# Kernel optimization log

Measured on AMD Instinct MI355X. Metric: run time of the kernel, lower is better.

Reference implementation:

```python
import jax, jax.numpy as jnp
import numpy as np

NUM_QUERIES = 150
NEG = 1e9


def setup_inputs() -> dict:
    key = jax.random.key(0)
    ks = jax.random.split(key, 5)
    B, C, H, W = 4, 256, 64, 64
    img_feat = jax.random.normal(ks[0], (B, C, H, W), dtype=jnp.float32)
    exe_feat = jax.random.normal(ks[1], (B, C), dtype=jnp.float32)
    mask = jax.random.bernoulli(ks[2], 0.9, (B, H, W)).astype(jnp.float32)
    # similarity initialized as identity (plus tiny noise so it's non-degenerate)
    similarity = jnp.eye(C, dtype=jnp.float32) + 0.01 * jax.random.normal(ks[3], (C, C), dtype=jnp.float32)
    # nn.Linear weight, shape (out, in)
    v_w = jax.random.normal(ks[4], (C, C), dtype=jnp.float32) / np.sqrt(C)
    return {"img_feat": img_feat, "exe_feat": exe_feat, "mask": mask,
            "similarity": similarity, "v_w": v_w}


def _get_queries(attn, B, H, W):
    # peak detection on similarity-to-exemplar channel (last column), no grad
    simil = jax.lax.stop_gradient(attn[:, :, -1]).reshape(B, H, W)
    c = simil[:, 1:-1, 1:-1]
    is_max = ((c > simil[:, :-2, 1:-1]) &   # strictly greater than above
              (c >= simil[:, 2:, 1:-1]) &   # >= below
              (c > simil[:, 1:-1, :-2]) &   # strictly greater than left
              (c >= simil[:, 1:-1, 2:]))    # >= right
    pen = jnp.zeros_like(simil).at[:, 1:-1, 1:-1].set(
        jnp.where(is_max, 0.0, NEG))
    scores = (simil - pen).reshape(B, H * W)
    _, q_ids = jax.lax.top_k(scores, NUM_QUERIES)  # [B, Q]
    return q_ids


def reference(img_feat, exe_feat, mask, similarity, v_w):
    B, C, H, W = img_feat.shape
    HW = H * W
    unrolled = img_feat.reshape(B, C, HW)                      # [B,C,HW]
    exe = (exe_feat * 1.2)[:, :, None]                         # [B,C,1]
    concat = jnp.concatenate([unrolled, exe], axis=2)          # [B,C,HW+1]
    # values = Linear(concat^T): x @ W^T
    values = jnp.einsum('bcn,dc->bnd', concat, v_w)            # [B,HW+1,C]
    # attn = unrolled^T @ similarity @ concat
    attn = jnp.einsum('bcn,cd,bdm->bnm', unrolled, similarity, concat)  # [B,HW,HW+1]

    q_ids = _get_queries(attn, B, H, W)                        # [B,Q] int
    queries = jnp.take_along_axis(values[:, :-1], q_ids[:, :, None], axis=1)  # [B,Q,C]

    # masked softmax: outer product of pixel mask, exemplar column always kept
    m = jax.lax.stop_gradient(mask).reshape(B, HW)
    mm = m[:, :, None] * m[:, None, :]                         # [B,HW,HW]
    mm = jnp.concatenate([mm, jnp.ones((B, HW, 1), mm.dtype)], axis=2)
    attn = attn - (mm != 1).astype(attn.dtype) * NEG
    attn = jax.nn.softmax(attn, axis=2)

    new_img = jnp.einsum('bnm,bmd->bnd', attn, values)         # [B,HW,C]
    new_img = new_img.transpose(0, 2, 1).reshape(B, C, H, W)
    return new_img + img_feat, queries
```

## Files before the change

kernel.cpp:

```cpp
#include <hip/hip_runtime.h>

#define CC   256
#define HWS  4096
#define MPAD 4160
#define NB   4
#define NTIL 65

typedef __attribute__((ext_vector_type(8))) short   short8;
typedef __attribute__((ext_vector_type(4))) float   floatx4;

static __device__ __forceinline__ short8 ld8(const unsigned short* p) {
  return *(const short8*)p;
}
static __device__ __forceinline__ void st8(unsigned short* p, short8 v) {
  *(short8*)p = v;
}
static __device__ __forceinline__ unsigned short f2b(float x) {
  union { float f; unsigned u; } v; v.f = x;
  unsigned r = v.u + 0x7FFFu + ((v.u >> 16) & 1u);
  return (unsigned short)(r >> 16);
}
static __device__ __forceinline__ float b2f(unsigned short x) {
  union { unsigned u; float f; } v; v.u = ((unsigned)x) << 16;
  return v.f;
}

__global__ void prep_colb(const float* __restrict__ sim, const float* __restrict__ vw,
                          const float* __restrict__ mask,
                          unsigned short* __restrict__ St, unsigned short* __restrict__ Vw,
                          float* __restrict__ colb) {
  int blk = blockIdx.x, tid = threadIdx.x;
  if (blk < CC) {
    int dd = blk, c = tid;
    St[dd*CC + c] = f2b(sim[c*CC + dd]);
    Vw[dd*CC + c] = f2b(vw[dd*CC + c]);
    return;
  }
  int b = blk - CC;
  for (int m = tid; m < MPAD; m += 256) {
    float v;
    if (m < HWS)      v = (mask[b*HWS + m] - 1.0f) * 1e9f;
    else if (m == HWS) v = 0.0f;
    else               v = -3.0e38f;
    colb[b*MPAD + m] = v;
  }
}

__global__ void build_kt(const float* __restrict__ img, const float* __restrict__ exe,
                         unsigned short* __restrict__ Kt, unsigned short* __restrict__ Kf) {
  int b = blockIdx.x, mt = blockIdx.y, dt = blockIdx.z;
  int tid = threadIdx.x;
  int m0 = mt*64, d0 = dt*64;
  int w = tid >> 6, lane = tid & 63, lo = lane & 15, hi = lane >> 4;
  unsigned short* kft = Kf + (size_t)(b*NTIL + mt)*16384;
  if (mt == 64) {
    for (int i = 0; i < 16; ++i) {
      int m = m0 + (tid>>6) + i*4;
      int d = d0 + (tid&63);
      unsigned short v = 0;
      if (m == 4096) v = f2b(1.2f * exe[b*CC + d]);
      Kt[((size_t)b*MPAD + m)*CC + d] = v;
    }
#pragma unroll
    for (int ss = 0; ss < 2; ++ss) {
      int s = dt*8 + w*2 + ss;
      int k = s >> 2, t = s & 3;
      unsigned short tmp[8] = {0,0,0,0,0,0,0,0};
      if (t == 0 && lo == 0) {
#pragma unroll
        for (int j = 0; j < 8; ++j)
          tmp[j] = f2b(1.2f * exe[b*CC + k*32 + hi*8 + j]);
      }
      st8(kft + s*512 + lane*8, *(short8*)tmp);
    }
    return;
  }
  __shared__ float tile[64][65];
  for (int i = 0; i < 16; ++i) {
    int dl = (tid>>6) + i*4, ml = tid&63;
    tile[dl][ml] = img[((size_t)b*CC + d0+dl)*HWS + m0+ml];
  }
  __syncthreads();
  for (int i = 0; i < 16; ++i) {
    int ml = (tid>>6) + i*4, dl = tid&63;
    Kt[((size_t)b*MPAD + m0+ml)*CC + d0+dl] = f2b(tile[dl][ml]);
  }
#pragma unroll
  for (int ss = 0; ss < 2; ++ss) {
    int s = dt*8 + w*2 + ss;
    int k = s >> 2, t = s & 3;
    int ml = t*16 + lo;
    int dlb = (k - dt*2)*32 + hi*8;
    unsigned short tmp[8];
#pragma unroll
    for (int j = 0; j < 8; ++j) tmp[j] = f2b(tile[dlb + j][ml]);
    st8(kft + s*512 + lane*8, *(short8*)tmp);
  }
}

__global__ __launch_bounds__(256) void gemm_small(const unsigned short* __restrict__ Kt,
    const unsigned short* __restrict__ Bm, unsigned short* __restrict__ Tout,
    unsigned short* __restrict__ Vf, int mode) {
  int b  = blockIdx.x;
  int by = blockIdx.y;
  int w  = threadIdx.x >> 6;
  int r0 = by*64 + w*16;
  int c0 = blockIdx.z*64;
  int lane = threadIdx.x & 63;
  int lo = lane & 15, hi = lane >> 4;
  __shared__ unsigned short lsh[64][72];
  floatx4 acc[4] = {};
  const unsigned short* arow = Kt + ((size_t)b*MPAD + r0 + lo)*CC + hi*8;
#pragma unroll
  for (int k = 0; k < 8; ++k) {
    short8 af = ld8(arow + k*32);
#pragma unroll
    for (int t = 0; t < 4; ++t) {
      short8 bf = ld8(Bm + (size_t)(c0 + t*16 + lo)*CC + k*32 + hi*8);
      acc[t] = __builtin_amdgcn_mfma_f32_16x16x32_bf16(af, bf, acc[t], 0, 0, 0);
    }
  }
  if (mode == 0) {
#pragma unroll
    for (int t = 0; t < 4; ++t)
#pragma unroll
      for (int r = 0; r < 4; ++r)
        lsh[w*16 + hi*4 + r][t*16 + lo] = f2b(acc[t][r]);
    __syncthreads();
    int tid = threadIdx.x;
    int nl = tid >> 2, seg = tid & 3;
    unsigned short* dst = Tout + ((size_t)b*HWS + by*64 + nl)*CC + c0 + seg*16;
    st8(dst,     ld8(&lsh[nl][seg*16]));
    st8(dst + 8, ld8(&lsh[nl][seg*16 + 8]));
  } else {
#pragma unroll
    for (int t = 0; t < 4; ++t)
#pragma unroll
      for (int r = 0; r < 4; ++r)
        lsh[t*16 + lo][w*16 + hi*4 + r] = f2b(acc[t][r]);
    __syncthreads();
    unsigned short* vfb2 = Vf + (size_t)(b*NTIL + by)*16384;
#pragma unroll
    for (int ss = 0; ss < 2; ++ss) {
      int idx = w*2 + ss;
      int h = idx >> 2, t4 = idx & 3;
      int s = h*16 + (c0 >> 4) + t4;
      short8 v = ld8(&lsh[t4*16 + (lane & 15)][h*32 + (lane >> 4)*8]);
      st8(vfb2 + s*512 + lane*8, v);
    }
  }
}

__global__ __launch_bounds__(256) void scores_kernel(const float* __restrict__ img,
    const float* __restrict__ sim, const float* __restrict__ exe,
    float* __restrict__ score32) {
  int b = blockIdx.x, n0 = blockIdx.y*32;
  int d = threadIdx.x;
  __shared__ float U[32][257];
  __shared__ float R[32][257];
  __shared__ float E[256];
  for (int idx = threadIdx.x; idx < 32*256; idx += 256) {
    int nl = idx & 31, c = idx >> 5;
    U[nl][c] = img[((size_t)b*CC + c)*HWS + n0 + nl];
  }
  E[d] = 1.2f * exe[b*CC + d];
  __syncthreads();
  float acc[32];
#pragma unroll
  for (int nl = 0; nl < 32; ++nl) acc[nl] = 0.f;
  for (int c = 0; c < CC; ++c) {
    float s_cd = sim[c*CC + d];
#pragma unroll
    for (int nl = 0; nl < 32; ++nl) acc[nl] = fmaf(U[nl][c], s_cd, acc[nl]);
  }
#pragma unroll
  for (int nl = 0; nl < 32; ++nl) R[nl][d] = acc[nl];
  __syncthreads();
  if (d < 32) {
    float s = 0.f;
    for (int dd = 0; dd < CC; ++dd) s = fmaf(R[d][dd], E[dd], s);
    score32[b*HWS + n0 + d] = s;
  }
}

__global__ __launch_bounds__(64) void select_kernel(const float* __restrict__ scores,
                                                    int* __restrict__ qids) {
  int b = blockIdx.x, lane = threadIdx.x;
  __shared__ float sc[HWS];
  __shared__ unsigned long long kx[HWS];
  __shared__ unsigned long long list[256];
  __shared__ unsigned int hist[256];
  __shared__ unsigned int st[4];
  __shared__ unsigned long long sh_base;

  const floatx4* s4 = (const floatx4*)(scores + (size_t)b*HWS);
  floatx4* c4 = (floatx4*)sc;
#pragma unroll
  for (int i = 0; i < 16; ++i) c4[i*64 + lane] = s4[i*64 + lane];
  __syncthreads();

  for (int i = 0; i < 64; ++i) {
    int idx = i*64 + lane;
    int y = i, x = lane;
    float c0 = sc[idx];
    float v = c0;
    if (y >= 1 && y <= 62 && x >= 1 && x <= 62) {
      bool ismax = (c0 > sc[idx-64]) && (c0 >= sc[idx+64]) &&
                   (c0 > sc[idx-1])  && (c0 >= sc[idx+1]);
      if (!ismax) v = c0 - 1e9f;
    }
    unsigned u = __float_as_uint(v);
    u = (u & 0x80000000u) ? ~u : (u | 0x80000000u);
    kx[idx] = (((unsigned long long)u) << 12) | (unsigned long long)(4095 - idx);
  }
  __syncthreads();

  unsigned long long base = 0;
  unsigned int need = 150, C = 0;
  for (int s = 36; s >= 4; s -= 8) {
    for (int i = lane; i < 256; i += 64) hist[i] = 0;
    __syncthreads();
    unsigned long long pref = base >> (s + 8);
    for (int i = 0; i < 64; ++i) {
      unsigned long long k = kx[i*64 + lane];
      if ((k >> (s + 8)) == pref) atomicAdd(&hist[(unsigned)(k >> s) & 255u], 1u);
    }
    __syncthreads();
    if (lane == 0) {
      unsigned cum = 0; int B = 0;
      for (int bin = 255; bin >= 0; --bin) {
        cum += hist[bin];
        if (cum >= need) { B = bin; break; }
      }
      st[0] = (150u - need) + cum;
      st[1] = need - (cum - hist[B]);
      sh_base = base | ((unsigned long long)B << s);
    }
    __syncthreads();
    C = st[0]; need = st[1]; base = sh_base;
    if (C <= 256u) break;
  }

  if (lane == 0) st[2] = 0;
  __syncthreads();
  for (int i = 0; i < 64; ++i) {
    unsigned long long k = kx[i*64 + lane];
    if (k >= base) {
      unsigned p = atomicAdd(&st[2], 1u);
      list[p] = k;
    }
  }
  __syncthreads();
  for (int i = lane; i < 256; i += 64) if (i >= (int)C) list[i] = 0ull;
  __syncthreads();

  for (int kk = 2; kk <= 256; kk <<= 1) {
    for (int j = kk >> 1; j > 0; j >>= 1) {
#pragma unroll
      for (int tt = 0; tt < 2; ++tt) {
        int t = lane + tt*64;
        int i2 = ((t & ~(j - 1)) << 1) | (t & (j - 1));
        int p2 = i2 | j;
        bool desc = ((i2 & kk) == 0);
        unsigned long long a = list[i2], c = list[p2];
        bool sw = desc ? (a < c) : (a > c);
        if (sw) { list[i2] = c; list[p2] = a; }
      }
      __syncthreads();
    }
  }

  for (int q = lane; q < 150; q += 64)
    qids[b*150 + q] = 4095 - (int)(list[q] & 0xFFFull);
}

__global__ __launch_bounds__(256, 1) void flash_kernel(
    const unsigned short* __restrict__ Tb, const unsigned short* __restrict__ Kt,
    const unsigned short* __restrict__ Kf, const unsigned short* __restrict__ Vf,
    const float* __restrict__ mask, const float* __restrict__ colb,
    float* __restrict__ acc0, float* __restrict__ accH, float* __restrict__ lsums) {
  int blk = blockIdx.x;
  int b    = (blk & 7) >> 1;
  int half = blk & 1;
  int g    = blk >> 3;
  int tid = threadIdx.x;
  int wave = tid >> 6, lane = tid & 63;
  int lo = lane & 15, hi = lane >> 4;
  int n0 = g*128 + wave*32;
  int t0 = half ? 33 : 0, t1 = half ? NTIL : 33;

  __shared__ unsigned short pbuf[4][1152];
  unsigned short* plw = &pbuf[wave][0];

  short8 q0[8], q1[8];
  const unsigned short* tb0 = Tb + ((size_t)b*HWS + n0 + lo)*CC + hi*8;
#pragma unroll
  for (int k = 0; k < 8; ++k) { q0[k] = ld8(tb0 + k*32); q1[k] = ld8(tb0 + 16*CC + k*32); }

  const unsigned short* kfb = Kf + (size_t)b*NTIL*16384 + lane*8;
  const unsigned short* vfb = Vf + (size_t)b*NTIL*16384 + lane*8;

  short8 X[16], Y[16];
#pragma unroll
  for (int i = 0; i < 16; ++i) X[i] = ld8(kfb + (size_t)t0*16384 + i*512);
#pragma unroll
  for (int i = 0; i < 16; ++i) Y[i] = ld8(kfb + (size_t)t0*16384 + (16 + i)*512);

  const float* mk = mask + b*HWS;

  float crb0[4], Msub0[4], crb1[4], Msub1[4];
  {
    const unsigned short* kep = Kt + ((size_t)b*MPAD + HWS)*CC + hi*8;
    float ddot = 0.f, edot = 0.f;
    const unsigned short* kdp = Kt + ((size_t)b*MPAD + n0 + lo)*CC + hi*8;
#pragma unroll
    for (int k = 0; k < 8; ++k) {
      short8 kd = ld8(kdp + k*32);
      short8 ke = ld8(kep + k*32);
#pragma unroll
      for (int j = 0; j < 8; ++j) {
        float qf = b2f((unsigned short)q0[k][j]);
        ddot = fmaf(qf, b2f((unsigned short)kd[j]), ddot);
        edot = fmaf(qf, b2f((unsigned short)ke[j]), edot);
      }
    }
    ddot += __shfl_xor(ddot, 16); ddot += __shfl_xor(ddot, 32);
    edot += __shfl_xor(edot, 16); edot += __shfl_xor(edot, 32);
    float Mrow = ((mk[n0 + lo] == 1.0f) ? ddot : edot) + 2.0f;
    float* fM = (float*)plw;
    fM[lo] = Mrow;
#pragma unroll
    for (int r = 0; r < 4; ++r) {
      Msub0[r] = fM[hi*4 + r];
      crb0[r]  = (mk[n0 + hi*4 + r] - 1.0f)*1e9f - Msub0[r];
    }
    ddot = 0.f; edot = 0.f;
    const unsigned short* kdp1 = Kt + ((size_t)b*MPAD + n0 + 16 + lo)*CC + hi*8;
#pragma unroll
    for (int k = 0; k < 8; ++k) {
      short8 kd = ld8(kdp1 + k*32);
      short8 ke = ld8(kep + k*32);
#pragma unroll
      for (int j = 0; j < 8; ++j) {
        float qf = b2f((unsigned short)q1[k][j]);
        ddot = fmaf(qf, b2f((unsigned short)kd[j]), ddot);
        edot = fmaf(qf, b2f((unsigned short)ke[j]), edot);
      }
    }
    ddot += __shfl_xor(ddot, 16); ddot += __shfl_xor(ddot, 32);
    edot += __shfl_xor(edot, 16); edot += __shfl_xor(edot, 32);
    float Mrow1 = ((mk[n0 + 16 + lo] == 1.0f) ? ddot : edot) + 2.0f;
    fM[lo] = Mrow1;
#pragma unroll
    for (int r = 0; r < 4; ++r) {
      Msub1[r] = fM[hi*4 + r];
      crb1[r]  = (mk[n0 + 16 + hi*4 + r] - 1.0f)*1e9f - Msub1[r];
    }
  }

  float lsum0[4] = {0.f, 0.f, 0.f, 0.f};
  float lsum1[4] = {0.f, 0.f, 0.f, 0.f};
  floatx4 o0[16] = {};
  floatx4 o1[16] = {};
  const float* cbb = colb + b*MPAD;

  for (int mt = t0; mt < t1; ++mt) {
    int m0 = mt*64;
    const unsigned short* vs = vfb + (size_t)mt*16384;
    floatx4 s0[4] = {}, s1[4] = {};
#pragma unroll
    for (int k = 0; k < 4; ++k)
#pragma unroll
      for (int t = 0; t < 4; ++t) {
        s0[t] = __builtin_amdgcn_mfma_f32_16x16x32_bf16(q0[k], X[k*4 + t], s0[t], 0, 0, 0);
        s1[t] = __builtin_amdgcn_mfma_f32_16x16x32_bf16(q1[k], X[k*4 + t], s1[t], 0, 0, 0);
      }
#pragma unroll
    for (int i = 0; i < 16; ++i) X[i] = ld8(vs + i*512);
#pragma unroll
    for (int k = 4; k < 8; ++k)
#pragma unroll
      for (int t = 0; t < 4; ++t) {
        s0[t] = __builtin_amdgcn_mfma_f32_16x16x32_bf16(q0[k], Y[(k-4)*4 + t], s0[t], 0, 0, 0);
        s1[t] = __builtin_amdgcn_mfma_f32_16x16x32_bf16(q1[k], Y[(k-4)*4 + t], s1[t], 0, 0, 0);
      }
#pragma unroll
    for (int i = 0; i < 16; ++i) Y[i] = ld8(vs + (16 + i)*512);
    float cb[4];
#pragma unroll
    for (int t = 0; t < 4; ++t) cb[t] = cbb[m0 + t*16 + lo];
    short8 pf00, pf01, pf10, pf11;
    {
      float pr[4][4];
#pragma unroll
      for (int t = 0; t < 4; ++t)
#pragma unroll
        for (int r = 0; r < 4; ++r)
          pr[t][r] = s0[t][r] + cb[t] + crb0[r];
      if (mt == NTIL-1 && lo == 0) {
#pragma unroll
        for (int r = 0; r < 4; ++r) pr[0][r] = s0[0][r] - Msub0[r];
      }
#pragma unroll
      for (int t = 0; t < 4; ++t)
#pragma unroll
        for (int r = 0; r < 4; ++r) {
          float p = __expf(pr[t][r]);
          lsum0[r] += p;
          plw[(hi*4 + r)*72 + t*16 + lo] = f2b(p);
        }
      pf00 = *(const short8*)&plw[lo*72 + hi*8];
      pf01 = *(const short8*)&plw[lo*72 + 32 + hi*8];
    }
    {
      float pr[4][4];
#pragma unroll
      for (int t = 0; t < 4; ++t)
#pragma unroll
        for (int r = 0; r < 4; ++r)
          pr[t][r] = s1[t][r] + cb[t] + crb1[r];
      if (mt == NTIL-1 && lo == 0) {
#pragma unroll
        for (int r = 0; r < 4; ++r) pr[0][r] = s1[0][r] - Msub1[r];
      }
#pragma unroll
      for (int t = 0; t < 4; ++t)
#pragma unroll
        for (int r = 0; r < 4; ++r) {
          float p = __expf(pr[t][r]);
          lsum1[r] += p;
          plw[(hi*4 + r)*72 + t*16 + lo] = f2b(p);
        }
      pf10 = *(const short8*)&plw[lo*72 + hi*8];
      pf11 = *(const short8*)&plw[lo*72 + 32 + hi*8];
    }
#pragma unroll
    for (int sl = 0; sl < 16; ++sl) {
      o0[sl] = __builtin_amdgcn_mfma_f32_16x16x32_bf16(pf00, X[sl], o0[sl], 0, 0, 0);
      o1[sl] = __builtin_amdgcn_mfma_f32_16x16x32_bf16(pf10, X[sl], o1[sl], 0, 0, 0);
    }
    if (mt + 1 < t1) {
      const unsigned short* ks = kfb + (size_t)(mt+1)*16384;
#pragma unroll
      for (int i = 0; i < 16; ++i) X[i] = ld8(ks + i*512);
    }
#pragma unroll
    for (int sl = 0; sl < 16; ++sl) {
      o0[sl] = __builtin_amdgcn_mfma_f32_16x16x32_bf16(pf01, Y[sl], o0[sl], 0, 0, 0);
      o1[sl] = __builtin_amdgcn_mfma_f32_16x16x32_bf16(pf11, Y[sl], o1[sl], 0, 0, 0);
    }
    if (mt + 1 < t1) {
      const unsigned short* ks = kfb + (size_t)(mt+1)*16384;
#pragma unroll
      for (int i = 0; i < 16; ++i) Y[i] = ld8(ks + (16 + i)*512);
    }
  }
#pragma unroll
  for (int r = 0; r < 4; ++r) {
#pragma unroll
    for (int off = 1; off < 16; off <<= 1) {
      lsum0[r] += __shfl_xor(lsum0[r], off);
      lsum1[r] += __shfl_xor(lsum1[r], off);
    }
  }
  float* op = (half ? accH : acc0) + (size_t)b*CC*HWS;
#pragma unroll
  for (int t = 0; t < 16; ++t)
#pragma unroll
    for (int r = 0; r < 4; ++r) {
      op[(size_t)(t*16 + lo)*HWS + n0 + hi*4 + r]      = o0[t][r];
      op[(size_t)(t*16 + lo)*HWS + n0 + 16 + hi*4 + r] = o1[t][r];
    }
  if (lo == 0) {
    float* lp = lsums + ((size_t)(half*NB + b))*HWS;
#pragma unroll
    for (int r = 0; r < 4; ++r) {
      lp[n0 + hi*4 + r]      = lsum0[r];
      lp[n0 + 16 + hi*4 + r] = lsum1[r];
    }
  }
}

__global__ __launch_bounds__(256) void finalize_kernel(const float* __restrict__ accH,
    const float* __restrict__ lsums, const float* __restrict__ img,
    float* __restrict__ out0) {
  int b = blockIdx.x >> 8;
  int d = blockIdx.x & 255;
  size_t base = ((size_t)b*CC + d)*HWS;
  const float* l0 = lsums + (size_t)b*HWS;
  const float* l1 = lsums + (size_t)(NB + b)*HWS;
  for (int n = threadIdx.x; n < HWS; n += 256) {
    float inv = 1.0f / (l0[n] + l1[n]);
    float o = (out0[base + n] + accH[base + n]) * inv;
    out0[base + n] = b2f(f2b(o)) + img[base + n];
  }
}

__global__ __launch_bounds__(256) void gather_kernel(const float* __restrict__ img,
    const float* __restrict__ vw, const int* __restrict__ qids, float* __restrict__ out1) {
  int blk = blockIdx.x;
  int b = blk / 150, q = blk % 150;
  int dd = threadIdx.x;
  __shared__ float col[CC];
  int id = qids[b*150 + q];
  col[dd] = img[((size_t)b*CC + dd)*HWS + id];
  __syncthreads();
  const float* vr = vw + dd*CC;
  float acc = 0.f;
  for (int c = 0; c < CC; ++c) acc = fmaf(col[c], vr[c], acc);
  out1[((size_t)(b*150 + q))*CC + dd] = acc;
}

extern "C" void kernel_launch(void* const* d_in, const int* in_sizes, int n_in,
                              void* d_out, int out_size, void* d_ws, size_t ws_size,
                              hipStream_t stream) {
  const float* img  = (const float*)d_in[0];
  const float* exe  = (const float*)d_in[1];
  const float* mask = (const float*)d_in[2];
  const float* sim  = (const float*)d_in[3];
  const float* vw   = (const float*)d_in[4];
  float* out0 = (float*)d_out;
  float* out1 = out0 + (size_t)NB*CC*HWS;

  char* ws = (char*)d_ws;
  size_t o = 0;
  unsigned short* Kt  = (unsigned short*)(ws + o); o += (size_t)NB*MPAD*CC*2;
  unsigned short* Tb  = (unsigned short*)(ws + o); o += (size_t)NB*HWS*CC*2;
  unsigned short* Kf  = (unsigned short*)(ws + o); o += (size_t)NB*NTIL*16384*2;
  unsigned short* Vf  = (unsigned short*)(ws + o); o += (size_t)NB*NTIL*16384*2;
  unsigned short* St  = (unsigned short*)(ws + o); o += (size_t)CC*CC*2;
  unsigned short* Vw  = (unsigned short*)(ws + o); o += (size_t)CC*CC*2;
  float*          scores = (float*)(ws + o);       o += (size_t)NB*HWS*4;
  float*          colb   = (float*)(ws + o);       o += (size_t)NB*MPAD*4;
  int*            qids   = (int*)(ws + o);         o += (size_t)NB*150*4;
  float*          accH   = (float*)(ws + o);       o += (size_t)NB*CC*HWS*4;
  float*          lsums  = (float*)(ws + o);       o += (size_t)2*NB*HWS*4;

  prep_colb  <<<dim3(CC + NB),    dim3(256), 0, stream>>>(sim, vw, mask, St, Vw, colb);
  build_kt   <<<dim3(NB, 65, 4),  dim3(256), 0, stream>>>(img, exe, Kt, Kf);
  gemm_small <<<dim3(NB, 64, 4),  dim3(256), 0, stream>>>(Kt, St, Tb, nullptr, 0);
  gemm_small <<<dim3(NB, 65, 4),  dim3(256), 0, stream>>>(Kt, Vw, nullptr, Vf, 1);
  scores_kernel<<<dim3(NB, 128),  dim3(256), 0, stream>>>(img, sim, exe, scores);
  select_kernel<<<dim3(NB),       dim3(64),  0, stream>>>(scores, qids);
  flash_kernel <<<dim3(256),      dim3(256), 0, stream>>>(Tb, Kt, Kf, Vf, mask, colb,
                                                          out0, accH, lsums);
  finalize_kernel<<<dim3(NB*CC),  dim3(256), 0, stream>>>(accH, lsums, img, out0);
  gather_kernel<<<dim3(NB*150),   dim3(256), 0, stream>>>(img, vw, qids, out1);
}
```

Before: 375.3 us.

## Split flash kernel key range across wave pairs and reduce partials in LDS

Each block now covers 64 query rows instead of 128. Its four waves form two row sets, and each pair of waves splits that half's key tiles in two. Partial outputs and row sums are combined through shared memory before the second wave writes them. The grid doubles to 512 blocks and launch bounds allow two blocks per CU, to raise occupancy and parallelism. In exchange it adds a large LDS buffer, several block barriers and the LDS reduction traffic, and the tighter launch bound may cause register spills given the large register arrays.

```diff
diff --git a/kernel.cpp b/kernel.cpp
--- a/kernel.cpp
+++ b/kernel.cpp
@@ -274,7 +274,7 @@
     qids[b*150 + q] = 4095 - (int)(list[q] & 0xFFFull);
 }
 
-__global__ __launch_bounds__(256, 1) void flash_kernel(
+__global__ __launch_bounds__(256, 2) void flash_kernel(
     const unsigned short* __restrict__ Tb, const unsigned short* __restrict__ Kt,
     const unsigned short* __restrict__ Kf, const unsigned short* __restrict__ Vf,
     const float* __restrict__ mask, const float* __restrict__ colb,
@@ -285,11 +285,17 @@
   int g    = blk >> 3;
   int tid = threadIdx.x;
   int wave = tid >> 6, lane = tid & 63;
+  int rowset = wave & 1;
+  int quart  = wave >> 1;
   int lo = lane & 15, hi = lane >> 4;
-  int n0 = g*128 + wave*32;
-  int t0 = half ? 33 : 0, t1 = half ? NTIL : 33;
+  int n0 = g*64 + rowset*32;
+  int h0 = half ? 33 : 0, h1 = half ? NTIL : 33;
+  int mid = (h0 + h1 + 1) >> 1;
+  int t0 = quart ? mid : h0;
+  int t1 = quart ? h1  : mid;
 
   __shared__ unsigned short pbuf[4][1152];
+  __shared__ float comb[2][64*65];
   unsigned short* plw = &pbuf[wave][0];
 
   short8 q0[8], q1[8];
@@ -455,6 +461,54 @@
       for (int i = 0; i < 16; ++i) Y[i] = ld8(ks + (16 + i)*512);
     }
   }
+
+  if (quart == 0) {
+#pragma unroll
+    for (int t = 0; t < 16; ++t)
+#pragma unroll
+      for (int r = 0; r < 4; ++r)
+        comb[rowset][lane*65 + t*4 + r] = o0[t][r];
+  }
+  __syncthreads();
+  if (quart == 1) {
+#pragma unroll
+    for (int t = 0; t < 16; ++t)
+#pragma unroll
+      for (int r = 0; r < 4; ++r)
+        o0[t][r] += comb[rowset][lane*65 + t*4 + r];
+  }
+  __syncthreads();
+  if (quart == 0) {
+#pragma unroll
+    for (int t = 0; t < 16; ++t)
+#pragma unroll
+      for (int r = 0; r < 4; ++r)
+        comb[rowset][lane*65 + t*4 + r] = o1[t][r];
+  }
+  __syncthreads();
+  if (quart == 1) {
+#pragma unroll
+    for (int t = 0; t < 16; ++t)
+#pragma unroll
+      for (int r = 0; r < 4; ++r)
+        o1[t][r] += comb[rowset][lane*65 + t*4 + r];
+  }
+  __syncthreads();
+  if (quart == 0) {
+#pragma unroll
+    for (int r = 0; r < 4; ++r) {
+      comb[rowset][lane*65 + r]     = lsum0[r];
+      comb[rowset][lane*65 + 4 + r] = lsum1[r];
+    }
+  }
+  __syncthreads();
+  if (quart == 0) return;
+#pragma unroll
+  for (int r = 0; r < 4; ++r) {
+    lsum0[r] += comb[rowset][lane*65 + r];
+    lsum1[r] += comb[rowset][lane*65 + 4 + r];
+  }
+
 #pragma unroll
   for (int r = 0; r < 4; ++r) {
 #pragma unroll
@@ -542,7 +596,7 @@
   gemm_small <<<dim3(NB, 65, 4),  dim3(256), 0, stream>>>(Kt, Vw, nullptr, Vf, 1);
   scores_kernel<<<dim3(NB, 128),  dim3(256), 0, stream>>>(img, sim, exe, scores);
   select_kernel<<<dim3(NB),       dim3(64),  0, stream>>>(scores, qids);
-  flash_kernel <<<dim3(256),      dim3(256), 0, stream>>>(Tb, Kt, Kf, Vf, mask, colb,
+  flash_kernel <<<dim3(512),      dim3(256), 0, stream>>>(Tb, Kt, Kf, Vf, mask, colb,
                                                           out0, accH, lsums);
   finalize_kernel<<<dim3(NB*CC),  dim3(256), 0, stream>>>(accH, lsums, img, out0);
   gather_kernel<<<dim3(NB*150),   dim3(256), 0, stream>>>(img, vw, qids, out1);
```

After: 809.0 us. 2.16x slower.
